# Kernel optimization log

Hardware: AMD Instinct MI355X
Metric: run time of the kernel (lower is better)

## Reference

```python
import jax, jax.numpy as jnp
import numpy as np
from jax import lax

T, B, I, H = 512, 64, 1024, 1024
MIN_VAL, MAX_VAL = -1.0, 1.0  # ConstScalarClamp bounds for both hardtanh norm-scales


def setup_inputs() -> dict:
    key = jax.random.key(0)
    ks = jax.random.split(key, 12)
    return {
        "inputs": jax.random.normal(ks[0], (T, B, I), jnp.float32),
        "state": jax.random.normal(ks[1], (B, H), jnp.float32),
        "weight_ri": jax.random.normal(ks[2], (H, I), jnp.float32) * 0.02,
        "weight_ii": jax.random.normal(ks[3], (H, I), jnp.float32) * 0.02,
        "weight_ni": jax.random.normal(ks[4], (H, I), jnp.float32) * 0.02,
        "weight_rh": jax.random.normal(ks[5], (H, H), jnp.float32) * 0.02,
        "weight_ih": jax.random.normal(ks[6], (H, H), jnp.float32) * 0.02,
        "weight_nh": jax.random.normal(ks[7], (H, H), jnp.float32) * 0.02,
        "bias_r": jax.random.normal(ks[8], (H,), jnp.float32) * 0.02,
        "bias_i": jax.random.normal(ks[9], (H,), jnp.float32) * 0.02,
        "bias_ni": jax.random.normal(ks[10], (H,), jnp.float32) * 0.02,
        "bias_nh": jax.random.normal(ks[11], (H,), jnp.float32) * 0.02,
    }


def _clamp(x):
    return jnp.clip(x, MIN_VAL, MAX_VAL)


def reference(inputs, state, weight_ri, weight_ii, weight_ni,
              weight_rh, weight_ih, weight_nh,
              bias_r, bias_i, bias_ni, bias_nh):
    # FP quant type: weight proxies are identity, quant_sigmoid/tanh are plain
    # sigmoid/tanh, and both norm-scale QuantHardTanh ops are clamp to [-1, 1].
    h0 = _clamp(state)  # state = norm_scale_out(state) before the loop

    def step(h, x_t):
        x = _clamp(x_t)  # input_quant = norm_scale_out(inputs[i])
        rgate = jax.nn.sigmoid(x @ weight_ri.T + h @ weight_rh.T + bias_r)
        igate = jax.nn.sigmoid(x @ weight_ii.T + h @ weight_ih.T + bias_i)
        gates_ni = x @ weight_ni.T + bias_ni
        gates_nh = h @ weight_nh.T + bias_nh
        ngate = jnp.tanh(_clamp(gates_ni) + _clamp(rgate * gates_nh))
        s = _clamp(h) - ngate
        hy = ngate + _clamp(igate * s)
        return hy, hy

    last, outputs = lax.scan(step, h0, inputs)
    return outputs, last
```

## Files before the change

### kernel.cpp

```cpp
#include <hip/hip_runtime.h>
#include <hip/hip_bf16.h>
#include <cstdio>


typedef short bf16x8 __attribute__((ext_vector_type(8)));
typedef float f32x4 __attribute__((ext_vector_type(4)));
typedef int i32x4 __attribute__((ext_vector_type(4)));

#define NT 512
#define NB 64
#define NH 1024
#define NBH 65536

#define OFF_HBUF  4096UL
#define OFF_WCAT  (OFF_HBUF + 2UL * NB * NH * 4)
#define OFF_WH    (OFF_WCAT + 3UL * NH * NH * 2)
#define OFF_GR    (OFF_WH   + 3UL * NH * NH * 2)
#define OFF_GI    (OFF_GR   + (unsigned long)NT * NB * NH * 2)
#define WS_NEED   (OFF_GI   + (unsigned long)NT * NB * NH * 2)

__device__ __forceinline__ float clampf(float x) { return fminf(fmaxf(x, -1.f), 1.f); }

__device__ __forceinline__ unsigned short f2bf(float x) {
  __hip_bfloat16 h = __float2bfloat16(x);
  union { __hip_bfloat16 h; unsigned short u; } cv;
  cv.h = h;
  return cv.u;
}
__device__ __forceinline__ float bf2f(unsigned short u) {
  return __uint_as_float(((unsigned)u) << 16);
}
__device__ __forceinline__ float frcp(float x) { return __builtin_amdgcn_rcpf(x); }
__device__ __forceinline__ float fsigmoid(float x) { return frcp(1.f + __expf(-x)); }
__device__ __forceinline__ float ftanh(float z) { return 1.f - 2.f * frcp(1.f + __expf(2.f * z)); }

__device__ __forceinline__ i32x4 pack8(float4 v0, float4 v1) {
  i32x4 q;
  q[0] = (int)(f2bf(clampf(v0.x)) | ((unsigned)f2bf(clampf(v0.y)) << 16));
  q[1] = (int)(f2bf(clampf(v0.z)) | ((unsigned)f2bf(clampf(v0.w)) << 16));
  q[2] = (int)(f2bf(clampf(v1.x)) | ((unsigned)f2bf(clampf(v1.y)) << 16));
  q[3] = (int)(f2bf(clampf(v1.z)) | ((unsigned)f2bf(clampf(v1.w)) << 16));
  return q;
}

__device__ __forceinline__ void gload_lds16(const void* g, void* l) {
  __builtin_amdgcn_global_load_lds(
      (const __attribute__((address_space(1))) void*)g,
      (__attribute__((address_space(3))) void*)l, 16, 0, 0);
}

__device__ __forceinline__ void load_frags8(const unsigned short* p, i32x4 a[8]) {
  asm volatile(
      "global_load_dwordx4 %0, %8, off\n\t"
      "global_load_dwordx4 %1, %8, off offset:64\n\t"
      "global_load_dwordx4 %2, %8, off offset:128\n\t"
      "global_load_dwordx4 %3, %8, off offset:192\n\t"
      "global_load_dwordx4 %4, %8, off offset:256\n\t"
      "global_load_dwordx4 %5, %8, off offset:320\n\t"
      "global_load_dwordx4 %6, %8, off offset:384\n\t"
      "global_load_dwordx4 %7, %8, off offset:448\n\t"
      "s_waitcnt vmcnt(0)"
      : "=&v"(a[0]), "=&v"(a[1]), "=&v"(a[2]), "=&v"(a[3]),
        "=&v"(a[4]), "=&v"(a[5]), "=&v"(a[6]), "=&v"(a[7])
      : "v"(p)
      : "memory");
}
__device__ __forceinline__ void store_u32_wt(unsigned int* p, unsigned v) {
  asm volatile("global_store_dword %0, %1, off sc0 sc1" :: "v"(p), "v"(v) : "memory");
}

__global__ void k_convert_weights(const float* __restrict__ wri, const float* __restrict__ wii,
                                  const float* __restrict__ wni, const float* __restrict__ wrh,
                                  const float* __restrict__ wih, const float* __restrict__ wnh,
                                  unsigned short* __restrict__ wcat, unsigned short* __restrict__ wh) {
  const long total = 6L * 1024 * 1024;
  long stride = (long)gridDim.x * blockDim.x * 4;
  for (long i = ((long)blockIdx.x * blockDim.x + threadIdx.x) * 4; i < total; i += stride) {
    int m = (int)(i >> 20);
    long off = i & 1048575L;
    const float* srcs[6] = {wri, wii, wni, wrh, wih, wnh};
    float4 v = *(const float4*)(srcs[m] + off);
    ushort4 o;
    o.x = f2bf(v.x); o.y = f2bf(v.y); o.z = f2bf(v.z); o.w = f2bf(v.w);
    unsigned short* dst = (m < 3) ? (wcat + ((long)m << 20) + off)
                                  : (wh + ((long)(m - 3) << 20) + off);
    *(ushort4*)dst = o;
  }
}

#define BK 64
__launch_bounds__(256)
__global__ void k_gemm_x(const float* __restrict__ A,
                         const unsigned short* __restrict__ Bw,
                         unsigned short* __restrict__ gr, unsigned short* __restrict__ gi,
                         float* __restrict__ gni,
                         const float* __restrict__ br, const float* __restrict__ bi,
                         const float* __restrict__ bni) {
  __shared__ unsigned short As[128 * BK];
  __shared__ unsigned short Bs[128 * BK];

  int bid = blockIdx.x;
  int bm = bid / 24, bn = bid % 24;
  int tid = threadIdx.x;
  int lane = tid & 63, w = tid >> 6;
  int wm = w >> 1, wn = w & 1;

  long arow0 = (long)bm * 128;
  long brow0 = (long)bn * 128;

  f32x4 acc[4][4] = {};

  for (int kt = 0; kt < 1024; kt += BK) {
    __syncthreads();
#pragma unroll
    for (int it = 0; it < 4; ++it) {
      int f = it * 2048 + tid * 8;
      int r = f >> 6, c = f & 63;
      gload_lds16(Bw + (brow0 + r) * 1024 + kt + c, &Bs[f]);
      const float* ap = A + (arow0 + r) * 1024 + kt + c;
      float4 v0 = *(const float4*)ap;
      float4 v1 = *(const float4*)(ap + 4);
      *(i32x4*)(&As[f]) = pack8(v0, v1);
    }
    __syncthreads();
#pragma unroll
    for (int ks = 0; ks < 2; ++ks) {
      bf16x8 a[4], b[4];
#pragma unroll
      for (int fm = 0; fm < 4; ++fm)
        a[fm] = *(const bf16x8*)(&As[(wm * 64 + fm * 16 + (lane & 15)) * BK + ks * 32 + (lane >> 4) * 8]);
#pragma unroll
      for (int fn = 0; fn < 4; ++fn)
        b[fn] = *(const bf16x8*)(&Bs[(wn * 64 + fn * 16 + (lane & 15)) * BK + ks * 32 + (lane >> 4) * 8]);
#pragma unroll
      for (int fm = 0; fm < 4; ++fm)
#pragma unroll
        for (int fn = 0; fn < 4; ++fn)
          acc[fm][fn] = __builtin_amdgcn_mfma_f32_16x16x32_bf16(a[fm], b[fn], acc[fm][fn], 0, 0, 0);
    }
  }

  int g = bn >> 3;
  const float* bias = (g == 0) ? br : (g == 1) ? bi : bni;
#pragma unroll
  for (int fm = 0; fm < 4; ++fm) {
    long m = arow0 + wm * 64 + fm * 16 + (lane >> 4) * 4;
#pragma unroll
    for (int fn = 0; fn < 4; ++fn) {
      long n = brow0 + wn * 64 + fn * 16 + (lane & 15);
      long colg = n & 1023;
      float bv = bias[colg];
#pragma unroll
      for (int r2 = 0; r2 < 4; ++r2) {
        float v = acc[fm][fn][r2] + bv;
        long idx = (m + r2) * 1024 + colg;
        if (g == 0)      gr[idx] = f2bf(v);
        else if (g == 1) gi[idx] = f2bf(v);
        else             gni[idx] = clampf(v);
      }
    }
  }
}

__launch_bounds__(512, 1)
__global__ void k_recurrent(const unsigned short* __restrict__ wh,
                            const unsigned short* __restrict__ gr,
                            const unsigned short* __restrict__ gi,
                            const float* __restrict__ state,
                            const float* __restrict__ bias_nh,
                            unsigned int* __restrict__ hbuf,
                            float* __restrict__ out) {
  __shared__ unsigned short h_lds[8 * 1024];
  __shared__ float red[4][3][2][2][8][16];

  int tid = threadIdx.x;
  int lane = tid & 63, w = tid >> 6;
  int ch = w >> 2;
  int kw = w & 3;
  int wg = blockIdx.x;
  int grp = wg >> 4;
  int slot = wg & 15;

  int klane = (lane >> 4) * 8;
  int k0 = kw * 256;
  i32x4 wfi[3][2][8];
#pragma unroll
  for (int g2 = 0; g2 < 3; ++g2)
#pragma unroll
    for (int n2 = 0; n2 < 2; ++n2) {
      int col = slot * 64 + ch * 32 + n2 * 16 + (lane & 15);
      load_frags8(wh + ((long)g2 << 20) + (long)col * 1024 + k0 + klane, wfi[g2][n2]);
    }

  int row = tid >> 6, col = tid & 63;
  long cellofs = (long)(grp * 8 + row) * 1024 + slot * 64 + col;
  float h_local = clampf(state[cellofs]);
  float bnh = bias_nh[slot * 64 + col];

#pragma unroll
  for (int c = 0; c < 4; ++c) {
    int n = c * 512 + tid;
    int r8 = n >> 8;
    int coli = (n * 4) & 1023;
    const float* sp = state + (long)(grp * 8 + r8) * 1024 + coli;
    float4 v = *(const float4*)sp;
    int2 pv;
    pv.x = (int)(f2bf(clampf(v.x)) | ((unsigned)f2bf(clampf(v.y)) << 16));
    pv.y = (int)(f2bf(clampf(v.z)) | ((unsigned)f2bf(clampf(v.w)) << 16));
    int flat = n * 8;
    *(int2*)((char*)h_lds + (flat ^ (r8 << 4))) = pv;
  }

  const int rowb = (lane & 7) * 2048;
  const int colb = kw * 512 + ((lane >> 4) * 16);
  const int rsw = (lane & 7) << 4;

  float grv = bf2f(gr[cellofs]);
  float giv = bf2f(gi[cellofs]);
  float gniv = out[cellofs];

  __syncthreads();

#pragma unroll 1
  for (int t = 0; t < NT; ++t) {
    f32x4 acc[3][2] = {};
#pragma unroll
    for (int s = 0; s < 8; ++s) {
      bf16x8 a = *(const bf16x8*)((const char*)h_lds + rowb + ((colb + s * 64) ^ rsw));
#pragma unroll
      for (int g2 = 0; g2 < 3; ++g2)
#pragma unroll
        for (int n2 = 0; n2 < 2; ++n2)
          acc[g2][n2] = __builtin_amdgcn_mfma_f32_16x16x32_bf16(
              a, __builtin_bit_cast(bf16x8, wfi[g2][n2][s]), acc[g2][n2], 0, 0, 0);
    }

    int rq = lane >> 4;
    if (rq < 2) {
#pragma unroll
      for (int g2 = 0; g2 < 3; ++g2)
#pragma unroll
        for (int n2 = 0; n2 < 2; ++n2)
#pragma unroll
          for (int r = 0; r < 4; ++r)
            red[kw][g2][n2][ch][rq * 4 + r][lane & 15] = acc[g2][n2][r];
    }
    __syncthreads();

    int chc = col >> 5, n2c = (col >> 4) & 1, cc = col & 15;
    float pr = red[0][0][n2c][chc][row][cc] + red[1][0][n2c][chc][row][cc]
             + red[2][0][n2c][chc][row][cc] + red[3][0][n2c][chc][row][cc];
    float pi = red[0][1][n2c][chc][row][cc] + red[1][1][n2c][chc][row][cc]
             + red[2][1][n2c][chc][row][cc] + red[3][1][n2c][chc][row][cc];
    float pn = red[0][2][n2c][chc][row][cc] + red[1][2][n2c][chc][row][cc]
             + red[2][2][n2c][chc][row][cc] + red[3][2][n2c][chc][row][cc];

    float rg = fsigmoid(pr + grv);
    float ig = fsigmoid(pi + giv);
    float ng = ftanh(gniv + clampf(rg * (pn + bnh)));
    float sx = clampf(h_local) - ng;
    float hy = ng + clampf(ig * sx);

    unsigned tgt = (unsigned)(t + 1);
    long bank = (long)(tgt & 1) * NBH;
    store_u32_wt(hbuf + bank + cellofs, ((unsigned)f2bf(hy) << 16) | tgt);
    out[(long)t * NBH + cellofs] = hy;
    h_local = hy;

    if (t + 1 < NT) {
      long g2ofs = (long)tgt * NBH + cellofs;
      grv = bf2f(gr[g2ofs]); giv = bf2f(gi[g2ofs]); gniv = out[g2ofs];

      const unsigned int* base = hbuf + bank + (long)grp * 8192;
      i32x4 d[4];
      for (unsigned it2 = 0;; ++it2) {
#pragma unroll
        for (int c = 0; c < 4; ++c) {
          const unsigned int* p = base + (long)(c * 512 + tid) * 4;
          asm volatile("global_load_dwordx4 %0, %1, off sc0 sc1"
                       : "=&v"(d[c]) : "v"(p) : "memory");
        }
        asm volatile("s_waitcnt vmcnt(0)" ::: "memory");
        unsigned mn = 0xFFFFFFFFu;
#pragma unroll
        for (int c = 0; c < 4; ++c)
#pragma unroll
          for (int e = 0; e < 4; ++e)
            mn = min(mn, ((unsigned)d[c][e]) & 0xFFFFu);
        if (__all((int)(mn >= tgt)) || it2 > 8192u) break;
        __builtin_amdgcn_s_sleep(1);
      }
#pragma unroll
      for (int c = 0; c < 4; ++c) {
        int n = c * 512 + tid;
        int r8 = n >> 8;
        int flat = n * 8;
        int2 v;
        v.x = (int)__builtin_amdgcn_perm((unsigned)d[c][1], (unsigned)d[c][0], 0x07060302u);
        v.y = (int)__builtin_amdgcn_perm((unsigned)d[c][3], (unsigned)d[c][2], 0x07060302u);
        *(int2*)((char*)h_lds + (flat ^ (r8 << 4))) = v;
      }
      __syncthreads();
    }
  }

  out[(long)NT * NBH + cellofs] = h_local;
}

extern "C" void kernel_launch(void* const* d_in, const int* in_sizes, int n_in,
                              void* d_out, int out_size, void* d_ws, size_t ws_size,
                              hipStream_t stream) {
  const float* inputs = (const float*)d_in[0];
  const float* state  = (const float*)d_in[1];
  const float* wri = (const float*)d_in[2];
  const float* wii = (const float*)d_in[3];
  const float* wni = (const float*)d_in[4];
  const float* wrh = (const float*)d_in[5];
  const float* wih = (const float*)d_in[6];
  const float* wnh = (const float*)d_in[7];
  const float* br  = (const float*)d_in[8];
  const float* bi  = (const float*)d_in[9];
  const float* bni = (const float*)d_in[10];
  const float* bnh = (const float*)d_in[11];

  if (ws_size < WS_NEED) {
    fprintf(stderr, "kernel_launch: ws too small (%zu < %lu)\n", ws_size, WS_NEED);
    return;
  }

  char* ws = (char*)d_ws;
  unsigned int*   hbuf  = (unsigned int*)(ws + OFF_HBUF);
  unsigned short* wcat  = (unsigned short*)(ws + OFF_WCAT);
  unsigned short* whp   = (unsigned short*)(ws + OFF_WH);
  unsigned short* grw   = (unsigned short*)(ws + OFF_GR);
  unsigned short* giw   = (unsigned short*)(ws + OFF_GI);
  float* out = (float*)d_out;

  hipMemsetAsync(ws, 0, OFF_WCAT, stream);
  k_convert_weights<<<512, 256, 0, stream>>>(wri, wii, wni, wrh, wih, wnh, wcat, whp);
  k_gemm_x<<<6144, 256, 0, stream>>>(inputs, wcat, grw, giw, out, br, bi, bni);
  k_recurrent<<<128, 512, 0, stream>>>(whp, grw, giw, state, bnh, hbuf, out);
}
```

Measured before the change: 1.757 ms.

## Have each recurrent block process two batch groups, halving grid size

The recurrent kernel now launches 64 blocks instead of 128. Each block handles two 8-row batch groups (A and B) with the same register-resident weight fragments, using separate LDS buffers and reduction arrays per group. This halves the number of blocks polling and synchronising through global memory on each timestep. The cost is twice the serial MFMA and epilogue work per block on each step, and half as many CUs in use.

Result: slower. 3.770 ms (+114.5%).

```diff
diff --git a/kernel.cpp b/kernel.cpp
--- a/kernel.cpp
+++ b/kernel.cpp
@@ -170,15 +170,18 @@
                             const float* __restrict__ bias_nh,
                             unsigned int* __restrict__ hbuf,
                             float* __restrict__ out) {
-  __shared__ unsigned short h_lds[8 * 1024];
-  __shared__ float red[4][3][2][2][8][16];
+  __shared__ unsigned short h_ldsA[8 * 1024];
+  __shared__ unsigned short h_ldsB[8 * 1024];
+  __shared__ float redA[4][3][2][2][8][16];
+  __shared__ float redB[4][3][2][2][8][16];
 
   int tid = threadIdx.x;
   int lane = tid & 63, w = tid >> 6;
   int ch = w >> 2;
   int kw = w & 3;
   int wg = blockIdx.x;
-  int grp = wg >> 4;
+  int gA = wg >> 4;
+  int gB = gA + 4;
   int slot = wg & 15;
 
   int klane = (lane >> 4) * 8;
@@ -193,8 +196,10 @@
     }
 
   int row = tid >> 6, col = tid & 63;
-  long cellofs = (long)(grp * 8 + row) * 1024 + slot * 64 + col;
-  float h_local = clampf(state[cellofs]);
+  long cellA = (long)(gA * 8 + row) * 1024 + slot * 64 + col;
+  long cellB = (long)(gB * 8 + row) * 1024 + slot * 64 + col;
+  float hA = clampf(state[cellA]);
+  float hB = clampf(state[cellB]);
   float bnh = bias_nh[slot * 64 + col];
 
 #pragma unroll
@@ -202,109 +207,202 @@
     int n = c * 512 + tid;
     int r8 = n >> 8;
     int coli = (n * 4) & 1023;
-    const float* sp = state + (long)(grp * 8 + r8) * 1024 + coli;
-    float4 v = *(const float4*)sp;
-    int2 pv;
-    pv.x = (int)(f2bf(clampf(v.x)) | ((unsigned)f2bf(clampf(v.y)) << 16));
-    pv.y = (int)(f2bf(clampf(v.z)) | ((unsigned)f2bf(clampf(v.w)) << 16));
     int flat = n * 8;
-    *(int2*)((char*)h_lds + (flat ^ (r8 << 4))) = pv;
+    int swz = flat ^ (r8 << 4);
+    {
+      const float* sp = state + (long)(gA * 8 + r8) * 1024 + coli;
+      float4 v = *(const float4*)sp;
+      int2 pv;
+      pv.x = (int)(f2bf(clampf(v.x)) | ((unsigned)f2bf(clampf(v.y)) << 16));
+      pv.y = (int)(f2bf(clampf(v.z)) | ((unsigned)f2bf(clampf(v.w)) << 16));
+      *(int2*)((char*)h_ldsA + swz) = pv;
+    }
+    {
+      const float* sp = state + (long)(gB * 8 + r8) * 1024 + coli;
+      float4 v = *(const float4*)sp;
+      int2 pv;
+      pv.x = (int)(f2bf(clampf(v.x)) | ((unsigned)f2bf(clampf(v.y)) << 16));
+      pv.y = (int)(f2bf(clampf(v.z)) | ((unsigned)f2bf(clampf(v.w)) << 16));
+      *(int2*)((char*)h_ldsB + swz) = pv;
+    }
   }
 
   const int rowb = (lane & 7) * 2048;
   const int colb = kw * 512 + ((lane >> 4) * 16);
   const int rsw = (lane & 7) << 4;
 
-  float grv = bf2f(gr[cellofs]);
-  float giv = bf2f(gi[cellofs]);
-  float gniv = out[cellofs];
+  float grvA = bf2f(gr[cellA]), givA = bf2f(gi[cellA]), gnivA = out[cellA];
+  float grvB = bf2f(gr[cellB]), givB = bf2f(gi[cellB]), gnivB = out[cellB];
 
   __syncthreads();
 
 #pragma unroll 1
   for (int t = 0; t < NT; ++t) {
-    f32x4 acc[3][2] = {};
-#pragma unroll
-    for (int s = 0; s < 8; ++s) {
-      bf16x8 a = *(const bf16x8*)((const char*)h_lds + rowb + ((colb + s * 64) ^ rsw));
-#pragma unroll
-      for (int g2 = 0; g2 < 3; ++g2)
-#pragma unroll
-        for (int n2 = 0; n2 < 2; ++n2)
-          acc[g2][n2] = __builtin_amdgcn_mfma_f32_16x16x32_bf16(
-              a, __builtin_bit_cast(bf16x8, wfi[g2][n2][s]), acc[g2][n2], 0, 0, 0);
-    }
-
-    int rq = lane >> 4;
-    if (rq < 2) {
-#pragma unroll
-      for (int g2 = 0; g2 < 3; ++g2)
-#pragma unroll
-        for (int n2 = 0; n2 < 2; ++n2)
-#pragma unroll
-          for (int r = 0; r < 4; ++r)
-            red[kw][g2][n2][ch][rq * 4 + r][lane & 15] = acc[g2][n2][r];
-    }
-    __syncthreads();
-
-    int chc = col >> 5, n2c = (col >> 4) & 1, cc = col & 15;
-    float pr = red[0][0][n2c][chc][row][cc] + red[1][0][n2c][chc][row][cc]
-             + red[2][0][n2c][chc][row][cc] + red[3][0][n2c][chc][row][cc];
-    float pi = red[0][1][n2c][chc][row][cc] + red[1][1][n2c][chc][row][cc]
-             + red[2][1][n2c][chc][row][cc] + red[3][1][n2c][chc][row][cc];
-    float pn = red[0][2][n2c][chc][row][cc] + red[1][2][n2c][chc][row][cc]
-             + red[2][2][n2c][chc][row][cc] + red[3][2][n2c][chc][row][cc];
-
-    float rg = fsigmoid(pr + grv);
-    float ig = fsigmoid(pi + giv);
-    float ng = ftanh(gniv + clampf(rg * (pn + bnh)));
-    float sx = clampf(h_local) - ng;
-    float hy = ng + clampf(ig * sx);
-
     unsigned tgt = (unsigned)(t + 1);
     long bank = (long)(tgt & 1) * NBH;
-    store_u32_wt(hbuf + bank + cellofs, ((unsigned)f2bf(hy) << 16) | tgt);
-    out[(long)t * NBH + cellofs] = hy;
-    h_local = hy;
+    int chc = col >> 5, n2c = (col >> 4) & 1, cc = col & 15;
+
+    {
+      f32x4 acc[3][2] = {};
+#pragma unroll
+      for (int s = 0; s < 8; ++s) {
+        bf16x8 a = *(const bf16x8*)((const char*)h_ldsA + rowb + ((colb + s * 64) ^ rsw));
+#pragma unroll
+        for (int g2 = 0; g2 < 3; ++g2)
+#pragma unroll
+          for (int n2 = 0; n2 < 2; ++n2)
+            acc[g2][n2] = __builtin_amdgcn_mfma_f32_16x16x32_bf16(
+                a, __builtin_bit_cast(bf16x8, wfi[g2][n2][s]), acc[g2][n2], 0, 0, 0);
+      }
+      int rq = lane >> 4;
+      if (rq < 2) {
+#pragma unroll
+        for (int g2 = 0; g2 < 3; ++g2)
+#pragma unroll
+          for (int n2 = 0; n2 < 2; ++n2)
+#pragma unroll
+            for (int r = 0; r < 4; ++r)
+              redA[kw][g2][n2][ch][rq * 4 + r][lane & 15] = acc[g2][n2][r];
+      }
+    }
+    __syncthreads();
+
+    {
+      float pr = redA[0][0][n2c][chc][row][cc] + redA[1][0][n2c][chc][row][cc]
+               + redA[2][0][n2c][chc][row][cc] + redA[3][0][n2c][chc][row][cc];
+      float pi = redA[0][1][n2c][chc][row][cc] + redA[1][1][n2c][chc][row][cc]
+               + redA[2][1][n2c][chc][row][cc] + redA[3][1][n2c][chc][row][cc];
+      float pn = redA[0][2][n2c][chc][row][cc] + redA[1][2][n2c][chc][row][cc]
+               + redA[2][2][n2c][chc][row][cc] + redA[3][2][n2c][chc][row][cc];
+      float rg = fsigmoid(pr + grvA);
+      float ig = fsigmoid(pi + givA);
+      float ng = ftanh(gnivA + clampf(rg * (pn + bnh)));
+      float sx = clampf(hA) - ng;
+      float hy = ng + clampf(ig * sx);
+      store_u32_wt(hbuf + bank + cellA, ((unsigned)f2bf(hy) << 16) | tgt);
+      out[(long)t * NBH + cellA] = hy;
+      hA = hy;
+      if (t + 1 < NT) {
+        long g2ofs = (long)tgt * NBH + cellA;
+        grvA = bf2f(gr[g2ofs]); givA = bf2f(gi[g2ofs]); gnivA = out[g2ofs];
+      }
+    }
+
+    {
+      f32x4 acc[3][2] = {};
+#pragma unroll
+      for (int s = 0; s < 8; ++s) {
+        bf16x8 a = *(const bf16x8*)((const char*)h_ldsB + rowb + ((colb + s * 64) ^ rsw));
+#pragma unroll
+        for (int g2 = 0; g2 < 3; ++g2)
+#pragma unroll
+          for (int n2 = 0; n2 < 2; ++n2)
+            acc[g2][n2] = __builtin_amdgcn_mfma_f32_16x16x32_bf16(
+                a, __builtin_bit_cast(bf16x8, wfi[g2][n2][s]), acc[g2][n2], 0, 0, 0);
+      }
+      int rq = lane >> 4;
+      if (rq < 2) {
+#pragma unroll
+        for (int g2 = 0; g2 < 3; ++g2)
+#pragma unroll
+          for (int n2 = 0; n2 < 2; ++n2)
+#pragma unroll
+            for (int r = 0; r < 4; ++r)
+              redB[kw][g2][n2][ch][rq * 4 + r][lane & 15] = acc[g2][n2][r];
+      }
+    }
+    __syncthreads();
+
+    {
+      float pr = redB[0][0][n2c][chc][row][cc] + redB[1][0][n2c][chc][row][cc]
+               + redB[2][0][n2c][chc][row][cc] + redB[3][0][n2c][chc][row][cc];
+      float pi = redB[0][1][n2c][chc][row][cc] + redB[1][1][n2c][chc][row][cc]
+               + redB[2][1][n2c][chc][row][cc] + redB[3][1][n2c][chc][row][cc];
+      float pn = redB[0][2][n2c][chc][row][cc] + redB[1][2][n2c][chc][row][cc]
+               + redB[2][2][n2c][chc][row][cc] + redB[3][2][n2c][chc][row][cc];
+      float rg = fsigmoid(pr + grvB);
+      float ig = fsigmoid(pi + givB);
+      float ng = ftanh(gnivB + clampf(rg * (pn + bnh)));
+      float sx = clampf(hB) - ng;
+      float hy = ng + clampf(ig * sx);
+      store_u32_wt(hbuf + bank + cellB, ((unsigned)f2bf(hy) << 16) | tgt);
+      out[(long)t * NBH + cellB] = hy;
+      hB = hy;
+      if (t + 1 < NT) {
+        long g2ofs = (long)tgt * NBH + cellB;
+        grvB = bf2f(gr[g2ofs]); givB = bf2f(gi[g2ofs]); gnivB = out[g2ofs];
+      }
+    }
 
     if (t + 1 < NT) {
-      long g2ofs = (long)tgt * NBH + cellofs;
-      grv = bf2f(gr[g2ofs]); giv = bf2f(gi[g2ofs]); gniv = out[g2ofs];
-
-      const unsigned int* base = hbuf + bank + (long)grp * 8192;
-      i32x4 d[4];
-      for (unsigned it2 = 0;; ++it2) {
+      {
+        const unsigned int* base = hbuf + bank + (long)gA * 8192;
+        i32x4 d[4];
+        for (unsigned it2 = 0;; ++it2) {
+#pragma unroll
+          for (int c = 0; c < 4; ++c) {
+            const unsigned int* p = base + (long)(c * 512 + tid) * 4;
+            asm volatile("global_load_dwordx4 %0, %1, off sc0 sc1"
+                         : "=&v"(d[c]) : "v"(p) : "memory");
+          }
+          asm volatile("s_waitcnt vmcnt(0)" ::: "memory");
+          unsigned mn = 0xFFFFFFFFu;
+#pragma unroll
+          for (int c = 0; c < 4; ++c)
+#pragma unroll
+            for (int e = 0; e < 4; ++e)
+              mn = min(mn, ((unsigned)d[c][e]) & 0xFFFFu);
+          if (__all((int)(mn >= tgt)) || it2 > 8192u) break;
+          __builtin_amdgcn_s_sleep(1);
+        }
 #pragma unroll
         for (int c = 0; c < 4; ++c) {
-          const unsigned int* p = base + (long)(c * 512 + tid) * 4;
-          asm volatile("global_load_dwordx4 %0, %1, off sc0 sc1"
-                       : "=&v"(d[c]) : "v"(p) : "memory");
+          int n = c * 512 + tid;
+          int r8 = n >> 8;
+          int flat = n * 8;
+          int2 v;
+          v.x = (int)__builtin_amdgcn_perm((unsigned)d[c][1], (unsigned)d[c][0], 0x07060302u);
+          v.y = (int)__builtin_amdgcn_perm((unsigned)d[c][3], (unsigned)d[c][2], 0x07060302u);
+          *(int2*)((char*)h_ldsA + (flat ^ (r8 << 4))) = v;
         }
-        asm volatile("s_waitcnt vmcnt(0)" ::: "memory");
-        unsigned mn = 0xFFFFFFFFu;
-#pragma unroll
-        for (int c = 0; c < 4; ++c)
-#pragma unroll
-          for (int e = 0; e < 4; ++e)
-            mn = min(mn, ((unsigned)d[c][e]) & 0xFFFFu);
-        if (__all((int)(mn >= tgt)) || it2 > 8192u) break;
-        __builtin_amdgcn_s_sleep(1);
-      }
-#pragma unroll
-      for (int c = 0; c < 4; ++c) {
-        int n = c * 512 + tid;
-        int r8 = n >> 8;
-        int flat = n * 8;
-        int2 v;
-        v.x = (int)__builtin_amdgcn_perm((unsigned)d[c][1], (unsigned)d[c][0], 0x07060302u);
-        v.y = (int)__builtin_amdgcn_perm((unsigned)d[c][3], (unsigned)d[c][2], 0x07060302u);
-        *(int2*)((char*)h_lds + (flat ^ (r8 << 4))) = v;
+      }
+      {
+        const unsigned int* base = hbuf + bank + (long)gB * 8192;
+        i32x4 d[4];
+        for (unsigned it2 = 0;; ++it2) {
+#pragma unroll
+          for (int c = 0; c < 4; ++c) {
+            const unsigned int* p = base + (long)(c * 512 + tid) * 4;
+            asm volatile("global_load_dwordx4 %0, %1, off sc0 sc1"
+                         : "=&v"(d[c]) : "v"(p) : "memory");
+          }
+          asm volatile("s_waitcnt vmcnt(0)" ::: "memory");
+          unsigned mn = 0xFFFFFFFFu;
+#pragma unroll
+          for (int c = 0; c < 4; ++c)
+#pragma unroll
+            for (int e = 0; e < 4; ++e)
+              mn = min(mn, ((unsigned)d[c][e]) & 0xFFFFu);
+          if (__all((int)(mn >= tgt)) || it2 > 8192u) break;
+          __builtin_amdgcn_s_sleep(1);
+        }
+#pragma unroll
+        for (int c = 0; c < 4; ++c) {
+          int n = c * 512 + tid;
+          int r8 = n >> 8;
+          int flat = n * 8;
+          int2 v;
+          v.x = (int)__builtin_amdgcn_perm((unsigned)d[c][1], (unsigned)d[c][0], 0x07060302u);
+          v.y = (int)__builtin_amdgcn_perm((unsigned)d[c][3], (unsigned)d[c][2], 0x07060302u);
+          *(int2*)((char*)h_ldsB + (flat ^ (r8 << 4))) = v;
+        }
       }
       __syncthreads();
     }
   }
 
-  out[(long)NT * NBH + cellofs] = h_local;
+  out[(long)NT * NBH + cellA] = hA;
+  out[(long)NT * NBH + cellB] = hB;
 }
 
 extern "C" void kernel_launch(void* const* d_in, const int* in_sizes, int n_in,
@@ -339,5 +437,5 @@
   hipMemsetAsync(ws, 0, OFF_WCAT, stream);
   k_convert_weights<<<512, 256, 0, stream>>>(wri, wii, wni, wrh, wih, wnh, wcat, whp);
   k_gemm_x<<<6144, 256, 0, stream>>>(inputs, wcat, grw, giw, out, br, bi, bni);
-  k_recurrent<<<128, 512, 0, stream>>>(whp, grw, giw, state, bnh, hbuf, out);
-}
+  k_recurrent<<<64, 512, 0, stream>>>(whp, grw, giw, state, bnh, hbuf, out);
+}
```

## Fuse input GEMM into recurrent kernel with per-row-block counters for overlap

Applied to the files above, without the earlier changes.

Merges the input-projection GEMM and the recurrent scan into one persistent launch. 128 workgroups run the recurrence while another 128 compute GEMM tiles and bump a per-row-block completion counter, so the scan can start before the whole projection is done. The recurrent workgroups spin on these counters, and they prefetch the next step's gate inputs before the hidden-state polling loop. The risks are that GEMM blocks compete with the latency-bound recurrence for CUs and bandwidth, that a smaller 128x64 tile with write-through stores lowers GEMM efficiency, and that correctness depends on all 256 blocks being co-resident.

Result: faster. 1.599 ms (-9.0%).

```diff
diff --git a/kernel.cpp b/kernel.cpp
--- a/kernel.cpp
+++ b/kernel.cpp
@@ -12,6 +12,7 @@
 #define NH 1024
 #define NBH 65536
 
+#define OFF_CNT   0UL
 #define OFF_HBUF  4096UL
 #define OFF_WCAT  (OFF_HBUF + 2UL * NB * NH * 4)
 #define OFF_WH    (OFF_WCAT + 3UL * NH * NH * 2)
@@ -67,6 +68,18 @@
 }
 __device__ __forceinline__ void store_u32_wt(unsigned int* p, unsigned v) {
   asm volatile("global_store_dword %0, %1, off sc0 sc1" :: "v"(p), "v"(v) : "memory");
+}
+__device__ __forceinline__ void store_u16_wt(unsigned short* p, unsigned v) {
+  asm volatile("global_store_short %0, %1, off sc0 sc1" :: "v"(p), "v"(v) : "memory");
+}
+__device__ __forceinline__ void store_f32_wt(float* p, float v) {
+  asm volatile("global_store_dword %0, %1, off sc0 sc1" :: "v"(p), "v"(v) : "memory");
+}
+__device__ __forceinline__ unsigned load_u32_mall(const unsigned int* p) {
+  unsigned v;
+  asm volatile("global_load_dword %0, %1, off sc0 sc1\n\ts_waitcnt vmcnt(0)"
+               : "=v"(v) : "v"(p) : "memory");
+  return v;
 }
 
 __global__ void k_convert_weights(const float* __restrict__ wri, const float* __restrict__ wii,
@@ -88,96 +101,95 @@
   }
 }
 
-#define BK 64
-__launch_bounds__(256)
-__global__ void k_gemm_x(const float* __restrict__ A,
-                         const unsigned short* __restrict__ Bw,
-                         unsigned short* __restrict__ gr, unsigned short* __restrict__ gi,
-                         float* __restrict__ gni,
-                         const float* __restrict__ br, const float* __restrict__ bi,
-                         const float* __restrict__ bni) {
-  __shared__ unsigned short As[128 * BK];
-  __shared__ unsigned short Bs[128 * BK];
-
-  int bid = blockIdx.x;
-  int bm = bid / 24, bn = bid % 24;
+__launch_bounds__(512, 1)
+__global__ void k_fused(const unsigned short* __restrict__ wh,
+                        const unsigned short* __restrict__ wcat,
+                        const float* __restrict__ X,
+                        const float* __restrict__ state,
+                        const float* __restrict__ br, const float* __restrict__ bi,
+                        const float* __restrict__ bni, const float* __restrict__ bnh,
+                        unsigned short* __restrict__ gr, unsigned short* __restrict__ gi,
+                        unsigned int* __restrict__ hbuf,
+                        unsigned int* __restrict__ cnt,
+                        float* __restrict__ out) {
+  __shared__ unsigned short h_lds[8 * 1024];
+  __shared__ float red[4][3][2][2][8][16];
+  __shared__ unsigned short As[128 * 64];
+  __shared__ unsigned short Bs[128 * 64];
+
   int tid = threadIdx.x;
   int lane = tid & 63, w = tid >> 6;
-  int wm = w >> 1, wn = w & 1;
-
-  long arow0 = (long)bm * 128;
-  long brow0 = (long)bn * 128;
-
-  f32x4 acc[4][4] = {};
-
-  for (int kt = 0; kt < 1024; kt += BK) {
-    __syncthreads();
-#pragma unroll
-    for (int it = 0; it < 4; ++it) {
-      int f = it * 2048 + tid * 8;
-      int r = f >> 6, c = f & 63;
-      gload_lds16(Bw + (brow0 + r) * 1024 + kt + c, &Bs[f]);
-      const float* ap = A + (arow0 + r) * 1024 + kt + c;
-      float4 v0 = *(const float4*)ap;
-      float4 v1 = *(const float4*)(ap + 4);
-      *(i32x4*)(&As[f]) = pack8(v0, v1);
-    }
-    __syncthreads();
-#pragma unroll
-    for (int ks = 0; ks < 2; ++ks) {
-      bf16x8 a[4], b[4];
-#pragma unroll
-      for (int fm = 0; fm < 4; ++fm)
-        a[fm] = *(const bf16x8*)(&As[(wm * 64 + fm * 16 + (lane & 15)) * BK + ks * 32 + (lane >> 4) * 8]);
-#pragma unroll
-      for (int fn = 0; fn < 4; ++fn)
-        b[fn] = *(const bf16x8*)(&Bs[(wn * 64 + fn * 16 + (lane & 15)) * BK + ks * 32 + (lane >> 4) * 8]);
-#pragma unroll
-      for (int fm = 0; fm < 4; ++fm)
-#pragma unroll
-        for (int fn = 0; fn < 4; ++fn)
-          acc[fm][fn] = __builtin_amdgcn_mfma_f32_16x16x32_bf16(a[fm], b[fn], acc[fm][fn], 0, 0, 0);
-    }
-  }
-
-  int g = bn >> 3;
-  const float* bias = (g == 0) ? br : (g == 1) ? bi : bni;
-#pragma unroll
-  for (int fm = 0; fm < 4; ++fm) {
-    long m = arow0 + wm * 64 + fm * 16 + (lane >> 4) * 4;
-#pragma unroll
-    for (int fn = 0; fn < 4; ++fn) {
-      long n = brow0 + wn * 64 + fn * 16 + (lane & 15);
-      long colg = n & 1023;
-      float bv = bias[colg];
-#pragma unroll
-      for (int r2 = 0; r2 < 4; ++r2) {
-        float v = acc[fm][fn][r2] + bv;
-        long idx = (m + r2) * 1024 + colg;
-        if (g == 0)      gr[idx] = f2bf(v);
-        else if (g == 1) gi[idx] = f2bf(v);
-        else             gni[idx] = clampf(v);
-      }
-    }
-  }
-}
-
-__launch_bounds__(512, 1)
-__global__ void k_recurrent(const unsigned short* __restrict__ wh,
-                            const unsigned short* __restrict__ gr,
-                            const unsigned short* __restrict__ gi,
-                            const float* __restrict__ state,
-                            const float* __restrict__ bias_nh,
-                            unsigned int* __restrict__ hbuf,
-                            float* __restrict__ out) {
-  __shared__ unsigned short h_lds[8 * 1024];
-  __shared__ float red[4][3][2][2][8][16];
-
-  int tid = threadIdx.x;
-  int lane = tid & 63, w = tid >> 6;
+  int wg = blockIdx.x;
+
+  if (wg >= 128) {
+    int gw = wg - 128;
+    int wm = w >> 2, wn = w & 3;
+    for (int i = 0; i < 48; ++i) {
+      int tile = i * 128 + gw;
+      int bm = tile / 24, bn = tile % 24;
+      long arow0 = (long)bm * 128;
+      long brow0 = (long)bn * 128;
+      f32x4 acc[4][2] = {};
+      for (int kt = 0; kt < 1024; kt += 64) {
+        __syncthreads();
+#pragma unroll
+        for (int it = 0; it < 2; ++it) {
+          int f = it * 4096 + tid * 8;
+          int r = f >> 6, c = f & 63;
+          gload_lds16(wcat + (brow0 + r) * 1024 + kt + c, &Bs[f]);
+          const float* ap = X + (arow0 + r) * 1024 + kt + c;
+          float4 v0 = *(const float4*)ap;
+          float4 v1 = *(const float4*)(ap + 4);
+          *(i32x4*)(&As[f]) = pack8(v0, v1);
+        }
+        __syncthreads();
+#pragma unroll
+        for (int ks = 0; ks < 2; ++ks) {
+          bf16x8 a[4], b[2];
+#pragma unroll
+          for (int fm = 0; fm < 4; ++fm)
+            a[fm] = *(const bf16x8*)(&As[(wm * 64 + fm * 16 + (lane & 15)) * 64 + ks * 32 + (lane >> 4) * 8]);
+#pragma unroll
+          for (int fn = 0; fn < 2; ++fn)
+            b[fn] = *(const bf16x8*)(&Bs[(wn * 32 + fn * 16 + (lane & 15)) * 64 + ks * 32 + (lane >> 4) * 8]);
+#pragma unroll
+          for (int fm = 0; fm < 4; ++fm)
+#pragma unroll
+            for (int fn = 0; fn < 2; ++fn)
+              acc[fm][fn] = __builtin_amdgcn_mfma_f32_16x16x32_bf16(a[fm], b[fn], acc[fm][fn], 0, 0, 0);
+        }
+      }
+      int g = bn >> 3;
+      const float* bias = (g == 0) ? br : (g == 1) ? bi : bni;
+#pragma unroll
+      for (int fm = 0; fm < 4; ++fm) {
+        long m = arow0 + wm * 64 + fm * 16 + (lane >> 4) * 4;
+#pragma unroll
+        for (int fn = 0; fn < 2; ++fn) {
+          long n = brow0 + wn * 32 + fn * 16 + (lane & 15);
+          long colg = n & 1023;
+          float bv = bias[colg];
+#pragma unroll
+          for (int r2 = 0; r2 < 4; ++r2) {
+            float v = acc[fm][fn][r2] + bv;
+            long idx = (m + r2) * 1024 + colg;
+            if (g == 0)      store_u16_wt(gr + idx, (unsigned)f2bf(v));
+            else if (g == 1) store_u16_wt(gi + idx, (unsigned)f2bf(v));
+            else             store_f32_wt(out + idx, clampf(v));
+          }
+        }
+      }
+      asm volatile("s_waitcnt vmcnt(0)" ::: "memory");
+      __syncthreads();
+      if (tid == 0)
+        __hip_atomic_fetch_add(&cnt[bm], 1u, __ATOMIC_RELAXED,
+                               __HIP_MEMORY_SCOPE_AGENT);
+    }
+    return;
+  }
+
   int ch = w >> 2;
   int kw = w & 3;
-  int wg = blockIdx.x;
   int grp = wg >> 4;
   int slot = wg & 15;
 
@@ -195,7 +207,7 @@
   int row = tid >> 6, col = tid & 63;
   long cellofs = (long)(grp * 8 + row) * 1024 + slot * 64 + col;
   float h_local = clampf(state[cellofs]);
-  float bnh = bias_nh[slot * 64 + col];
+  float bnh_v = bnh[slot * 64 + col];
 
 #pragma unroll
   for (int c = 0; c < 4; ++c) {
@@ -215,9 +227,27 @@
   const int colb = kw * 512 + ((lane >> 4) * 16);
   const int rsw = (lane & 7) << 4;
 
-  float grv = bf2f(gr[cellofs]);
-  float giv = bf2f(gi[cellofs]);
-  float gniv = out[cellofs];
+  {
+    unsigned it = 0;
+    while (load_u32_mall(&cnt[0]) < 24u && it < (1u << 17)) {
+      ++it;
+      __builtin_amdgcn_s_sleep(8);
+    }
+  }
+  float grv, giv, gniv;
+  {
+    unsigned a, b; float c;
+    asm volatile(
+        "global_load_ushort %0, %3, off sc0 sc1\n\t"
+        "global_load_ushort %1, %4, off sc0 sc1\n\t"
+        "global_load_dword %2, %5, off sc0 sc1\n\t"
+        "s_waitcnt vmcnt(0)"
+        : "=&v"(a), "=&v"(b), "=&v"(c)
+        : "v"(gr + cellofs), "v"(gi + cellofs), "v"(out + cellofs)
+        : "memory");
+    grv = bf2f((unsigned short)a); giv = bf2f((unsigned short)b); gniv = c;
+  }
+  unsigned wm_done = 1;
 
   __syncthreads();
 
@@ -257,7 +287,7 @@
 
     float rg = fsigmoid(pr + grv);
     float ig = fsigmoid(pi + giv);
-    float ng = ftanh(gniv + clampf(rg * (pn + bnh)));
+    float ng = ftanh(gniv + clampf(rg * (pn + bnh_v)));
     float sx = clampf(h_local) - ng;
     float hy = ng + clampf(ig * sx);
 
@@ -268,8 +298,25 @@
     h_local = hy;
 
     if (t + 1 < NT) {
+      unsigned bm_needed = tgt >> 1;
+      if (bm_needed >= wm_done) {
+        unsigned it = 0;
+        while (load_u32_mall(&cnt[bm_needed]) < 24u && it < (1u << 17)) {
+          ++it;
+          __builtin_amdgcn_s_sleep(8);
+        }
+        wm_done = bm_needed + 1;
+      }
+
       long g2ofs = (long)tgt * NBH + cellofs;
-      grv = bf2f(gr[g2ofs]); giv = bf2f(gi[g2ofs]); gniv = out[g2ofs];
+      unsigned pwa, pwb; float pwc;
+      asm volatile(
+          "global_load_ushort %0, %3, off sc0 sc1\n\t"
+          "global_load_ushort %1, %4, off sc0 sc1\n\t"
+          "global_load_dword %2, %5, off sc0 sc1"
+          : "=&v"(pwa), "=&v"(pwb), "=&v"(pwc)
+          : "v"(gr + g2ofs), "v"(gi + g2ofs), "v"(out + g2ofs)
+          : "memory");
 
       const unsigned int* base = hbuf + bank + (long)grp * 8192;
       i32x4 d[4];
@@ -290,6 +337,11 @@
         if (__all((int)(mn >= tgt)) || it2 > 8192u) break;
         __builtin_amdgcn_s_sleep(1);
       }
+      __builtin_amdgcn_sched_barrier(0);
+      grv = bf2f((unsigned short)pwa);
+      giv = bf2f((unsigned short)pwb);
+      gniv = pwc;
+
 #pragma unroll
       for (int c = 0; c < 4; ++c) {
         int n = c * 512 + tid;
@@ -329,6 +381,7 @@
   }
 
   char* ws = (char*)d_ws;
+  unsigned int*   cnt   = (unsigned int*)(ws + OFF_CNT);
   unsigned int*   hbuf  = (unsigned int*)(ws + OFF_HBUF);
   unsigned short* wcat  = (unsigned short*)(ws + OFF_WCAT);
   unsigned short* whp   = (unsigned short*)(ws + OFF_WH);
@@ -338,6 +391,6 @@
 
   hipMemsetAsync(ws, 0, OFF_WCAT, stream);
   k_convert_weights<<<512, 256, 0, stream>>>(wri, wii, wni, wrh, wih, wnh, wcat, whp);
-  k_gemm_x<<<6144, 256, 0, stream>>>(inputs, wcat, grw, giw, out, br, bi, bni);
-  k_recurrent<<<128, 512, 0, stream>>>(whp, grw, giw, state, bnh, hbuf, out);
-}
+  k_fused<<<256, 512, 0, stream>>>(whp, wcat, inputs, state, br, bi, bni, bnh,
+                                   grw, giw, hbuf, cnt, out);
+}
```
